# Optimization experiments

Hardware: AMD Instinct MI355X
Metric: run time of the kernel (lower is better)

Reference implementation:

```python
import jax, jax.numpy as jnp
import numpy as np

T, NE, NA, OBS, D, CH, VH, ITERS = 128, 64, 8, 64, 128, 128, 256, 2
B = NE * NA  # num_actors


def setup_inputs() -> dict:
    key = jax.random.key(0)
    ks = jax.random.split(key, 16)
    rn = lambda k, shape, s=0.05: jax.random.normal(k, shape, jnp.float32) * s
    z = lambda *shape: jnp.zeros(shape, jnp.float32)
    return dict(
        hidden=z(B, D),
        obs=rn(ks[0], (T, B, OBS), 1.0),
        dones=jax.random.bernoulli(ks[1], 0.05, (T, B)),
        embed1_w=rn(ks[2], (OBS, D)), embed1_b=z(D),
        embed2_w=rn(ks[3], (D, D)), embed2_b=z(D),
        gru_Wi=rn(ks[4], (D, 3 * D)), gru_bi=z(3 * D),
        gru_Wh=rn(ks[5], (D, 3 * D)), gru_bhn=z(D),
        couple_h_w=rn(ks[6], (2 * D, CH)), couple_h_b=z(CH),
        couple_out_w=rn(ks[7], (CH, 1)), couple_out_b=z(1),
        update_h_w=rn(ks[8], (2 * D, D)), update_h_b=z(D),
        update_out_w=rn(ks[9], (D, D)), update_out_b=z(D),
        value_h1_w=rn(ks[10], (D, VH)), value_h1_b=z(VH),
        value_h2_w=rn(ks[11], (VH, VH)), value_h2_b=z(VH),
        value_out_w=rn(ks[12], (VH, 1)), value_out_b=z(1),
    )


def _gru_scan(hidden, x, dones, Wi, bi, Wh, bhn):
    # flax GRUCell math: r,z gates (no hidden bias), n gate with hidden bias.
    def step(h, xd):
        xt, dt = xd
        h = jnp.where(dt[:, None], 0.0, h)  # reset carry on done
        gi = xt @ Wi + bi                   # [B, 3D]
        gh = h @ Wh                         # [B, 3D]
        i_r, i_z, i_n = jnp.split(gi, 3, axis=-1)
        h_r, h_z, h_n = jnp.split(gh, 3, axis=-1)
        r = jax.nn.sigmoid(i_r + h_r)
        zg = jax.nn.sigmoid(i_z + h_z)
        n = jnp.tanh(i_n + r * (h_n + bhn))
        new_h = (1.0 - zg) * n + zg * h
        return new_h, new_h
    return jax.lax.scan(step, hidden, (x, dones))


def reference(hidden, obs, dones,
              embed1_w, embed1_b, embed2_w, embed2_b,
              gru_Wi, gru_bi, gru_Wh, gru_bhn,
              couple_h_w, couple_h_b, couple_out_w, couple_out_b,
              update_h_w, update_h_b, update_out_w, update_out_b,
              value_h1_w, value_h1_b, value_h2_w, value_h2_b,
              value_out_w, value_out_b):
    # observation embedding MLP
    emb = jax.nn.relu(obs @ embed1_w + embed1_b)
    emb = jax.nn.relu(emb @ embed2_w + embed2_b)
    hidden, rnn_out = _gru_scan(hidden, emb, dones, gru_Wi, gru_bi, gru_Wh, gru_bhn)

    e = rnn_out.reshape(T, NE, NA, D)
    alive = (1.0 - dones.astype(jnp.float32)).reshape(T, NE, NA)
    e = e * alive[..., None]
    identity_mask = 1.0 - jnp.eye(NA, dtype=jnp.float32)

    # split-linear trick: couple_h(concat[h_i, h_j]) == h_i @ W1 + h_j @ W2 + b
    W1, W2 = couple_h_w[:D], couple_h_w[D:]
    U1, U2 = update_h_w[:D], update_h_w[D:]

    for _ in range(ITERS):
        a_i = jnp.einsum('teid,dh->teih', e, W1)  # [T,E,A,CH]
        a_j = jnp.einsum('tejd,dh->tejh', e, W2)
        Ch = jax.nn.relu(a_i[:, :, :, None, :] + a_j[:, :, None, :, :] + couple_h_b)  # [T,E,A,A,CH]
        C = jax.nn.sigmoid(jnp.einsum('teijh,h->teij', Ch, couple_out_w[:, 0]) + couple_out_b[0])
        C = C * alive[:, :, None, :] * identity_mask[None, None, :, :]
        context = jnp.einsum('teij,tejd->teid', C, e)
        delta = jax.nn.relu(e @ U1 + context @ U2 + update_h_b)
        delta = jax.nn.relu(delta @ update_out_w + update_out_b)
        e = (e + delta) * alive[..., None]

    v = jax.nn.relu(e @ value_h1_w + value_h1_b)
    v = jax.nn.relu(v @ value_h2_w + value_h2_b)
    v = (v @ value_out_w + value_out_b)[..., 0]  # [T,E,A]
    values = v.reshape(T, B)
    return hidden, values
```

## Files before the change

### kernel.cpp

```cpp
#include <hip/hip_runtime.h>
#include <hip/hip_bf16.h>
#include <math.h>

#define T_ 128
#define NE_ 64
#define NA_ 8
#define B_ 512
#define OBS_ 64
#define D_ 128
#define CH_ 128
#define VH_ 256
#define M_ (T_*B_)

typedef __attribute__((ext_vector_type(8))) short bf16x8;
typedef __attribute__((ext_vector_type(8))) _Float16 f16x8;
typedef __attribute__((ext_vector_type(4))) float f32x4;

__device__ __forceinline__ float sigmoidf_(float x){ return 1.f/(1.f+__expf(-x)); }
__device__ __forceinline__ unsigned short f2bu(float v){
  __hip_bfloat16 b = __float2bfloat16(v);
  return __builtin_bit_cast(unsigned short, b);
}
__device__ __forceinline__ float bu2f(unsigned short u){
  return __builtin_bit_cast(float, (unsigned int)u << 16);
}
__device__ __forceinline__ unsigned short f2hu(float v){
  _Float16 h = (_Float16)v;
  return __builtin_bit_cast(unsigned short, h);
}
__device__ __forceinline__ float hu2f(unsigned short u){
  return (float)__builtin_bit_cast(_Float16, u);
}

__global__ __launch_bounds__(256)
void embgi_k(const float* __restrict__ obs,
             const ushort* __restrict__ e1wT, const float* __restrict__ e1b,
             const ushort* __restrict__ e2wT, const float* __restrict__ e2b,
             const ushort* __restrict__ gWiT, const float* __restrict__ gbi,
             ushort* __restrict__ giH)
{
  __shared__ ushort S1[128*136];
  __shared__ ushort S2[128*136];
  const int tid  = threadIdx.x;
  const int lane = tid & 63, wave = tid >> 6;
  const int wm = wave >> 1, wn = wave & 1;
  const int quad = lane >> 4, ln = lane & 15;
  const int m0 = blockIdx.x * 128;

  f32x4 acc[4][4];

  #pragma unroll
  for (int i=0;i<8;i++){
    int c4 = tid + i*256;
    int m = c4 >> 4, kf = (c4 & 15) * 4;
    float4 v = *(const float4*)&obs[(size_t)(m0+m)*OBS_ + kf];
    ushort4 h; h.x=f2hu(v.x); h.y=f2hu(v.y); h.z=f2hu(v.z); h.w=f2hu(v.w);
    *(ushort4*)&S1[m*136 + kf] = h;
  }
  #pragma unroll
  for (int i=0;i<4;i++){
    int c8 = tid + i*256;
    int n = c8 >> 3, kq = (c8 & 7)*8;
    *(uint4*)&S2[n*136 + kq] = *(const uint4*)&e1wT[(size_t)n*64 + kq];
  }
  __syncthreads();

  #pragma unroll
  for (int i=0;i<4;i++)
    #pragma unroll
    for (int j=0;j<4;j++)
      #pragma unroll
      for (int r=0;r<4;r++) acc[i][j][r] = 0.f;
  #pragma unroll
  for (int ks=0; ks<2; ks++){
    const int kq = ks*32 + quad*8;
    f16x8 af[4], bfv[4];
    #pragma unroll
    for (int mt=0;mt<4;mt++)
      af[mt] = *(const f16x8*)&S1[(wm*64 + mt*16 + ln)*136 + kq];
    #pragma unroll
    for (int nt=0;nt<4;nt++)
      bfv[nt] = *(const f16x8*)&S2[(wn*64 + nt*16 + ln)*136 + kq];
    #pragma unroll
    for (int mt=0;mt<4;mt++)
      #pragma unroll
      for (int nt=0;nt<4;nt++)
        acc[mt][nt] = __builtin_amdgcn_mfma_f32_16x16x32_f16(af[mt], bfv[nt], acc[mt][nt], 0,0,0);
  }
  __syncthreads();

  #pragma unroll
  for (int mt=0;mt<4;mt++)
    #pragma unroll
    for (int r=0;r<4;r++){
      int rl = wm*64 + mt*16 + quad*4 + r;
      #pragma unroll
      for (int nt=0;nt<4;nt++){
        int cl = wn*64 + nt*16 + ln;
        S1[rl*136 + cl] = f2hu(fmaxf(acc[mt][nt][r] + e1b[cl], 0.f));
      }
    }
  #pragma unroll
  for (int i=0;i<8;i++){
    int c8 = tid + i*256;
    int n = c8 >> 4, kq = (c8 & 15)*8;
    *(uint4*)&S2[n*136 + kq] = *(const uint4*)&e2wT[(size_t)n*128 + kq];
  }
  __syncthreads();

  #pragma unroll
  for (int i=0;i<4;i++)
    #pragma unroll
    for (int j=0;j<4;j++)
      #pragma unroll
      for (int r=0;r<4;r++) acc[i][j][r] = 0.f;
  #pragma unroll
  for (int ks=0; ks<4; ks++){
    const int kq = ks*32 + quad*8;
    f16x8 af[4], bfv[4];
    #pragma unroll
    for (int mt=0;mt<4;mt++)
      af[mt] = *(const f16x8*)&S1[(wm*64 + mt*16 + ln)*136 + kq];
    #pragma unroll
    for (int nt=0;nt<4;nt++)
      bfv[nt] = *(const f16x8*)&S2[(wn*64 + nt*16 + ln)*136 + kq];
    #pragma unroll
    for (int mt=0;mt<4;mt++)
      #pragma unroll
      for (int nt=0;nt<4;nt++)
        acc[mt][nt] = __builtin_amdgcn_mfma_f32_16x16x32_f16(af[mt], bfv[nt], acc[mt][nt], 0,0,0);
  }
  __syncthreads();

  #pragma unroll
  for (int mt=0;mt<4;mt++)
    #pragma unroll
    for (int r=0;r<4;r++){
      int rl = wm*64 + mt*16 + quad*4 + r;
      #pragma unroll
      for (int nt=0;nt<4;nt++){
        int cl = wn*64 + nt*16 + ln;
        S1[rl*136 + cl] = f2hu(fmaxf(acc[mt][nt][r] + e2b[cl], 0.f));
      }
    }

  for (int c=0; c<3; c++){
    #pragma unroll
    for (int i=0;i<8;i++){
      int c8 = tid + i*256;
      int n = c8 >> 4, kq = (c8 & 15)*8;
      *(uint4*)&S2[n*136 + kq] = *(const uint4*)&gWiT[(size_t)(c*128+n)*128 + kq];
    }
    __syncthreads();
    #pragma unroll
    for (int i=0;i<4;i++)
      #pragma unroll
      for (int j=0;j<4;j++)
        #pragma unroll
        for (int r=0;r<4;r++) acc[i][j][r] = 0.f;
    #pragma unroll
    for (int ks=0; ks<4; ks++){
      const int kq = ks*32 + quad*8;
      f16x8 af[4], bfv[4];
      #pragma unroll
      for (int mt=0;mt<4;mt++)
        af[mt] = *(const f16x8*)&S1[(wm*64 + mt*16 + ln)*136 + kq];
      #pragma unroll
      for (int nt=0;nt<4;nt++)
        bfv[nt] = *(const f16x8*)&S2[(wn*64 + nt*16 + ln)*136 + kq];
      #pragma unroll
      for (int mt=0;mt<4;mt++)
        #pragma unroll
        for (int nt=0;nt<4;nt++)
          acc[mt][nt] = __builtin_amdgcn_mfma_f32_16x16x32_f16(af[mt], bfv[nt], acc[mt][nt], 0,0,0);
    }
    __syncthreads();
    #pragma unroll
    for (int mt=0;mt<4;mt++)
      #pragma unroll
      for (int r=0;r<4;r++){
        int row = m0 + wm*64 + mt*16 + quad*4 + r;
        #pragma unroll
        for (int nt=0;nt<4;nt++){
          int cl = wn*64 + nt*16 + ln;
          giH[(size_t)row*384 + c*128 + cl] = f2hu(acc[mt][nt][r] + gbi[c*128 + cl]);
        }
      }
  }
}

__global__ __launch_bounds__(512, 1)
void postgru_k(const __hip_bfloat16* __restrict__ Xe, const __hip_bfloat16* __restrict__ bcatT,
               const float* __restrict__ chb, const float* __restrict__ cow,
               const float* __restrict__ cob,
               const __hip_bfloat16* __restrict__ uhwT, const float* __restrict__ uhb,
               const __hip_bfloat16* __restrict__ uowT, const float* __restrict__ uob,
               const int* __restrict__ dones,
               const __hip_bfloat16* __restrict__ v1wT, const float* __restrict__ v1b,
               const __hip_bfloat16* __restrict__ v2wT, const float* __restrict__ v2b,
               const float* __restrict__ vow, const float* __restrict__ vob,
               float* __restrict__ values)
{
  __shared__ ushort S1[128*136];
  __shared__ ushort Bs[128*136];
  __shared__ alignas(16) ushort Pool[2*128*136];
  __shared__ alignas(16) float cbw[CH_], cww[CH_];
  __shared__ float Cs[4][NA_][NA_];
  __shared__ float SRed[128];
  const int tid  = threadIdx.x;
  const int lane = tid & 63, wave = tid >> 6;
  const int wm = wave >> 1, wn = wave & 1;
  const int quad = lane >> 4, ln = lane & 15;
  const int m0 = blockIdx.x * 128;

  ushort* XcS = Pool;
  float (*AI)[132] = (float(*)[132])(Pool + 128*136);
  float (*AJ)[132] = (float(*)[132])((char*)(Pool + 128*136) + 16896);

  #pragma unroll
  for (int i=0;i<4;i++){
    int c8 = tid + i*512;
    int m = c8 >> 4, kq = (c8 & 15)*8;
    *(uint4*)&S1[m*136 + kq] = *(const uint4*)((const ushort*)Xe + (size_t)(m0+m)*128 + kq);
  }
  if (tid < 128){ cbw[tid] = chb[tid]; cww[tid] = cow[tid]; }
  const float cob0 = cob[0];
  __syncthreads();

  for (int it=0; it<2; it++){
    for (int g=0; g<4; g++){
      const int r0 = g*32;
      const int wrow = wave >> 2;
      const int wcol = wave & 3;

      #pragma unroll
      for (int i=0;i<4;i++){
        int c8 = tid + i*512;
        int n = c8 >> 4, kq = (c8 & 15)*8;
        *(uint4*)&Bs[n*136 + kq] = *(const uint4*)((const ushort*)bcatT + (size_t)n*128 + kq);
      }
      __syncthreads();
      {
        f32x4 accc[2];
        #pragma unroll
        for (int nt=0;nt<2;nt++)
          #pragma unroll
          for (int r=0;r<4;r++) accc[nt][r] = 0.f;
        #pragma unroll
        for (int ks=0; ks<4; ks++){
          const int kq = ks*32 + quad*8;
          bf16x8 af = *(const bf16x8*)&S1[(r0 + wrow*16 + ln)*136 + kq];
          #pragma unroll
          for (int nt=0;nt<2;nt++){
            bf16x8 bfv = *(const bf16x8*)&Bs[(wcol*32 + nt*16 + ln)*136 + kq];
            accc[nt] = __builtin_amdgcn_mfma_f32_16x16x32_bf16(af, bfv, accc[nt], 0,0,0);
          }
        }
        __syncthreads();
        #pragma unroll
        for (int nt=0;nt<2;nt++)
          #pragma unroll
          for (int r=0;r<4;r++)
            AI[wrow*16 + quad*4 + r][wcol*32 + nt*16 + ln] = accc[nt][r];
      }
      #pragma unroll
      for (int i=0;i<4;i++){
        int c8 = tid + i*512;
        int n = c8 >> 4, kq = (c8 & 15)*8;
        *(uint4*)&Bs[n*136 + kq] = *(const uint4*)((const ushort*)bcatT + (size_t)(128+n)*128 + kq);
      }
      __syncthreads();
      {
        f32x4 accc[2];
        #pragma unroll
        for (int nt=0;nt<2;nt++)
          #pragma unroll
          for (int r=0;r<4;r++) accc[nt][r] = 0.f;
        #pragma unroll
        for (int ks=0; ks<4; ks++){
          const int kq = ks*32 + quad*8;
          bf16x8 af = *(const bf16x8*)&S1[(r0 + wrow*16 + ln)*136 + kq];
          #pragma unroll
          for (int nt=0;nt<2;nt++){
            bf16x8 bfv = *(const bf16x8*)&Bs[(wcol*32 + nt*16 + ln)*136 + kq];
            accc[nt] = __builtin_amdgcn_mfma_f32_16x16x32_bf16(af, bfv, accc[nt], 0,0,0);
          }
        }
        #pragma unroll
        for (int nt=0;nt<2;nt++)
          #pragma unroll
          for (int r=0;r<4;r++)
            AJ[wrow*16 + quad*4 + r][wcol*32 + nt*16 + ln] = accc[nt][r];
      }
      __syncthreads();

      {
        const int env = tid >> 7;
        const int i   = (tid >> 4) & 7;
        const int jg  = (tid >> 3) & 1;
        const int hq  = tid & 7;
        const float* aiR = &AI[env*8 + i][0];
        const float* aj0 = &AJ[env*8 + jg*4 + 0][0];
        const float* aj1 = &AJ[env*8 + jg*4 + 1][0];
        const float* aj2 = &AJ[env*8 + jg*4 + 2][0];
        const float* aj3 = &AJ[env*8 + jg*4 + 3][0];
        float s0=0.f, s1=0.f, s2=0.f, s3=0.f;
        #pragma unroll
        for (int t=0; t<4; t++){
          int h = (hq + t*8)*4;
          float4 a4 = *(const float4*)&aiR[h];
          float4 c4 = *(const float4*)&cbw[h];
          float4 w4 = *(const float4*)&cww[h];
          float px = a4.x + c4.x, py = a4.y + c4.y, pz = a4.z + c4.z, pw = a4.w + c4.w;
          float4 b0 = *(const float4*)&aj0[h];
          s0 += fmaxf(px+b0.x,0.f)*w4.x + fmaxf(py+b0.y,0.f)*w4.y
              + fmaxf(pz+b0.z,0.f)*w4.z + fmaxf(pw+b0.w,0.f)*w4.w;
          float4 b1 = *(const float4*)&aj1[h];
          s1 += fmaxf(px+b1.x,0.f)*w4.x + fmaxf(py+b1.y,0.f)*w4.y
              + fmaxf(pz+b1.z,0.f)*w4.z + fmaxf(pw+b1.w,0.f)*w4.w;
          float4 b2 = *(const float4*)&aj2[h];
          s2 += fmaxf(px+b2.x,0.f)*w4.x + fmaxf(py+b2.y,0.f)*w4.y
              + fmaxf(pz+b2.z,0.f)*w4.z + fmaxf(pw+b2.w,0.f)*w4.w;
          float4 b3 = *(const float4*)&aj3[h];
          s3 += fmaxf(px+b3.x,0.f)*w4.x + fmaxf(py+b3.y,0.f)*w4.y
              + fmaxf(pz+b3.z,0.f)*w4.z + fmaxf(pw+b3.w,0.f)*w4.w;
        }
        s0 += __shfl_xor(s0,1); s0 += __shfl_xor(s0,2); s0 += __shfl_xor(s0,4);
        s1 += __shfl_xor(s1,1); s1 += __shfl_xor(s1,2); s1 += __shfl_xor(s1,4);
        s2 += __shfl_xor(s2,1); s2 += __shfl_xor(s2,2); s2 += __shfl_xor(s2,4);
        s3 += __shfl_xor(s3,1); s3 += __shfl_xor(s3,2); s3 += __shfl_xor(s3,4);
        if (hq == 0){
          int j0 = jg*4;
          float c0 = sigmoidf_(s0 + cob0); Cs[env][i][j0+0] = (i==j0+0)?0.f:c0;
          float c1 = sigmoidf_(s1 + cob0); Cs[env][i][j0+1] = (i==j0+1)?0.f:c1;
          float c2 = sigmoidf_(s2 + cob0); Cs[env][i][j0+2] = (i==j0+2)?0.f:c2;
          float c3 = sigmoidf_(s3 + cob0); Cs[env][i][j0+3] = (i==j0+3)?0.f:c3;
        }
      }
      __syncthreads();

      {
        const int lr = tid >> 4;
        const int env = lr >> 3, ii = lr & 7;
        const int c0 = (tid & 15) * 8;
        #pragma unroll
        for (int cc=0; cc<2; cc++){
          int d = c0 + cc*4;
          float a0=0.f, a1=0.f, a2=0.f, a3=0.f;
          #pragma unroll
          for (int j=0;j<NA_;j++){
            float c = Cs[env][ii][j];
            ushort4 e4 = *(const ushort4*)&S1[(r0 + env*8 + j)*136 + d];
            a0 = fmaf(c, bu2f(e4.x), a0);
            a1 = fmaf(c, bu2f(e4.y), a1);
            a2 = fmaf(c, bu2f(e4.z), a2);
            a3 = fmaf(c, bu2f(e4.w), a3);
          }
          ushort4 o; o.x=f2bu(a0); o.y=f2bu(a1); o.z=f2bu(a2); o.w=f2bu(a3);
          *(ushort4*)&XcS[(r0 + lr)*136 + d] = o;
        }
      }
      __syncthreads();
    }

    f32x4 acc[2][4];
    #pragma unroll
    for (int i=0;i<2;i++)
      #pragma unroll
      for (int j=0;j<4;j++)
        #pragma unroll
        for (int r=0;r<4;r++) acc[i][j][r] = 0.f;

    #pragma unroll
    for (int kc=0; kc<2; kc++){
      #pragma unroll
      for (int i=0;i<4;i++){
        int c8 = tid + i*512;
        int n = c8 >> 4, kq = (c8 & 15)*8;
        *(uint4*)&Bs[n*136 + kq] = *(const uint4*)((const ushort*)uhwT + (size_t)n*256 + kc*128 + kq);
      }
      __syncthreads();
      const ushort* Ab = kc ? XcS : S1;
      #pragma unroll
      for (int ks=0; ks<4; ks++){
        const int kq = ks*32 + quad*8;
        bf16x8 af[2], bfv[4];
        #pragma unroll
        for (int mt=0;mt<2;mt++)
          af[mt] = *(const bf16x8*)&Ab[(wm*32 + mt*16 + ln)*136 + kq];
        #pragma unroll
        for (int nt=0;nt<4;nt++)
          bfv[nt] = *(const bf16x8*)&Bs[(wn*64 + nt*16 + ln)*136 + kq];
        #pragma unroll
        for (int mt=0;mt<2;mt++)
          #pragma unroll
          for (int nt=0;nt<4;nt++)
            acc[mt][nt] = __builtin_amdgcn_mfma_f32_16x16x32_bf16(af[mt], bfv[nt], acc[mt][nt], 0,0,0);
      }
      __syncthreads();
    }

    #pragma unroll
    for (int i=0;i<4;i++){
      int c8 = tid + i*512;
      int n = c8 >> 4, kq = (c8 & 15)*8;
      *(uint4*)&Bs[n*136 + kq] = *(const uint4*)((const ushort*)uowT + (size_t)n*128 + kq);
    }
    #pragma unroll
    for (int mt=0;mt<2;mt++)
      #pragma unroll
      for (int r=0;r<4;r++){
        int rl = wm*32 + mt*16 + quad*4 + r;
        #pragma unroll
        for (int nt=0;nt<4;nt++){
          int cl = wn*64 + nt*16 + ln;
          XcS[rl*136 + cl] = f2bu(fmaxf(acc[mt][nt][r] + uhb[cl], 0.f));
        }
      }
    __syncthreads();

    f32x4 acc2[2][4];
    #pragma unroll
    for (int i=0;i<2;i++)
      #pragma unroll
      for (int j=0;j<4;j++)
        #pragma unroll
        for (int r=0;r<4;r++) acc2[i][j][r] = 0.f;
    #pragma unroll
    for (int ks=0; ks<4; ks++){
      const int kq = ks*32 + quad*8;
      bf16x8 af[2], bfv[4];
      #pragma unroll
      for (int mt=0;mt<2;mt++)
        af[mt] = *(const bf16x8*)&XcS[(wm*32 + mt*16 + ln)*136 + kq];
      #pragma unroll
      for (int nt=0;nt<4;nt++)
        bfv[nt] = *(const bf16x8*)&Bs[(wn*64 + nt*16 + ln)*136 + kq];
      #pragma unroll
      for (int mt=0;mt<2;mt++)
        #pragma unroll
        for (int nt=0;nt<4;nt++)
          acc2[mt][nt] = __builtin_amdgcn_mfma_f32_16x16x32_bf16(af[mt], bfv[nt], acc2[mt][nt], 0,0,0);
    }
    #pragma unroll
    for (int mt=0;mt<2;mt++){
      #pragma unroll
      for (int r=0;r<4;r++){
        int rl = wm*32 + mt*16 + quad*4 + r;
        int row = m0 + rl;
        float al = (dones[row]!=0) ? 0.f : 1.f;
        #pragma unroll
        for (int nt=0;nt<4;nt++){
          int cl = wn*64 + nt*16 + ln;
          float v = fmaxf(acc2[mt][nt][r] + uob[cl], 0.f);
          v += bu2f(S1[rl*136 + cl]);
          v *= al;
          S1[rl*136 + cl] = f2bu(v);
        }
      }
    }
    __syncthreads();
  }

  ushort* V1 = Pool;

  for (int h=0; h<2; h++){
    #pragma unroll
    for (int i=0;i<4;i++){
      int c8 = tid + i*512;
      int n = c8 >> 4, kq = (c8 & 15)*8;
      *(uint4*)&Bs[n*136 + kq] = *(const uint4*)((const ushort*)v1wT + (size_t)(h*128+n)*128 + kq);
    }
    __syncthreads();
    f32x4 acc[2][4];
    #pragma unroll
    for (int i=0;i<2;i++)
      #pragma unroll
      for (int j=0;j<4;j++)
        #pragma unroll
        for (int r=0;r<4;r++) acc[i][j][r] = 0.f;
    #pragma unroll
    for (int ks=0; ks<4; ks++){
      const int kq = ks*32 + quad*8;
      bf16x8 af[2], bfv[4];
      #pragma unroll
      for (int mt=0;mt<2;mt++)
        af[mt] = *(const bf16x8*)&S1[(wm*32 + mt*16 + ln)*136 + kq];
      #pragma unroll
      for (int nt=0;nt<4;nt++)
        bfv[nt] = *(const bf16x8*)&Bs[(wn*64 + nt*16 + ln)*136 + kq];
      #pragma unroll
      for (int mt=0;mt<2;mt++)
        #pragma unroll
        for (int nt=0;nt<4;nt++)
          acc[mt][nt] = __builtin_amdgcn_mfma_f32_16x16x32_bf16(af[mt], bfv[nt], acc[mt][nt], 0,0,0);
    }
    __syncthreads();
    #pragma unroll
    for (int mt=0;mt<2;mt++)
      #pragma unroll
      for (int r=0;r<4;r++){
        int rl = wm*32 + mt*16 + quad*4 + r;
        #pragma unroll
        for (int nt=0;nt<4;nt++){
          int cl = wn*64 + nt*16 + ln;
          V1[h*128*136 + rl*136 + cl] = f2bu(fmaxf(acc[mt][nt][r] + v1b[h*128 + cl], 0.f));
        }
      }
  }

  float s[2][4];
  #pragma unroll
  for (int mt=0;mt<2;mt++)
    #pragma unroll
    for (int r=0;r<4;r++) s[mt][r] = 0.f;

  for (int oc=0; oc<2; oc++){
    f32x4 acc[2][4];
    #pragma unroll
    for (int i=0;i<2;i++)
      #pragma unroll
      for (int j=0;j<4;j++)
        #pragma unroll
        for (int r=0;r<4;r++) acc[i][j][r] = 0.f;
    for (int kh=0; kh<2; kh++){
      #pragma unroll
      for (int i=0;i<4;i++){
        int c8 = tid + i*512;
        int n = c8 >> 4, kq = (c8 & 15)*8;
        *(uint4*)&Bs[n*136 + kq] = *(const uint4*)((const ushort*)v2wT + (size_t)(oc*128+n)*256 + kh*128 + kq);
      }
      __syncthreads();
      #pragma unroll
      for (int ks=0; ks<4; ks++){
        const int kq = ks*32 + quad*8;
        bf16x8 af[2], bfv[4];
        #pragma unroll
        for (int mt=0;mt<2;mt++)
          af[mt] = *(const bf16x8*)&V1[kh*128*136 + (wm*32 + mt*16 + ln)*136 + kq];
        #pragma unroll
        for (int nt=0;nt<4;nt++)
          bfv[nt] = *(const bf16x8*)&Bs[(wn*64 + nt*16 + ln)*136 + kq];
        #pragma unroll
        for (int mt=0;mt<2;mt++)
          #pragma unroll
          for (int nt=0;nt<4;nt++)
            acc[mt][nt] = __builtin_amdgcn_mfma_f32_16x16x32_bf16(af[mt], bfv[nt], acc[mt][nt], 0,0,0);
      }
      __syncthreads();
    }
    float v2bv[4], voww[4];
    #pragma unroll
    for (int nt=0;nt<4;nt++){
      int col = oc*128 + wn*64 + nt*16 + ln;
      v2bv[nt] = v2b[col];
      voww[nt] = vow[col];
    }
    #pragma unroll
    for (int mt=0;mt<2;mt++)
      #pragma unroll
      for (int r=0;r<4;r++){
        float p = 0.f;
        #pragma unroll
        for (int nt=0;nt<4;nt++)
          p += fmaxf(acc[mt][nt][r] + v2bv[nt], 0.f) * voww[nt];
        s[mt][r] += p;
      }
  }

  #pragma unroll
  for (int off=1; off<16; off<<=1)
    #pragma unroll
    for (int mt=0;mt<2;mt++)
      #pragma unroll
      for (int r=0;r<4;r++)
        s[mt][r] += __shfl_xor(s[mt][r], off);
  if (ln == 0 && wn == 1){
    #pragma unroll
    for (int mt=0;mt<2;mt++)
      #pragma unroll
      for (int r=0;r<4;r++)
        SRed[wm*32 + mt*16 + quad*4 + r] = s[mt][r];
  }
  __syncthreads();
  if (ln == 0 && wn == 0){
    float vob0 = vob[0];
    #pragma unroll
    for (int mt=0;mt<2;mt++)
      #pragma unroll
      for (int r=0;r<4;r++){
        int rl = wm*32 + mt*16 + quad*4 + r;
        values[m0 + rl] = s[mt][r] + SRed[rl] + vob0;
      }
  }
}

__global__ __launch_bounds__(512, 1)
void grum8_k(const ushort* __restrict__ gih, const float* __restrict__ hidden0,
             const int* __restrict__ dones, const float* __restrict__ gWh,
             const float* __restrict__ bhn, __hip_bfloat16* __restrict__ eb_out,
             float* __restrict__ hout)
{
  __shared__ ushort wstg[32*392];
  __shared__ ushort hb[2][16*136];
  __shared__ float  dnS[T_*4];
  const int tid  = threadIdx.x;
  const int lane = tid & 63, wave = tid >> 6;
  const int quad = lane >> 4, ln = lane & 15;
  const int r0   = blockIdx.x * 4;
  const int col  = wave*16 + ln;
  const int lnb  = ln & 12;

  dnS[tid] = (dones[(size_t)(tid>>2)*B_ + r0 + (tid&3)] != 0) ? 1.f : 0.f;
  const float bhnr = bhn[col];

  for (int i=tid; i<16*136; i+=512){ hb[0][i]=0; hb[1][i]=0; }

  f16x8 bf[3][4];
  #pragma unroll
  for (int kc=0; kc<4; kc++){
    for (int i=tid; i<32*384; i+=512){
      int kk = i/384, c = i - kk*384;
      wstg[kk*392 + c] = f2hu(gWh[(size_t)(kc*32+kk)*384 + c]);
    }
    __syncthreads();
    #pragma unroll
    for (int g=0; g<3; g++){
      int c = g*128 + col;
      ushort tmp[8];
      #pragma unroll
      for (int j=0;j<8;j++) tmp[j] = wstg[(quad*8+j)*392 + c];
      bf[g][kc] = *(const f16x8*)tmp;
    }
    __syncthreads();
  }

  float hc = hidden0[(size_t)(r0+quad)*D_ + col];
  if (dnS[quad] > 0.5f) hc = 0.f;
  hb[0][(quad*4)*136 + col] = f2hu(hc);
  __syncthreads();

  const ushort* gbase = gih + ((size_t)(r0+quad))*384;
  const size_t  gstep = (size_t)B_*384;

  float c_r, c_z, c_n;
  c_r = hu2f(gbase[col]); c_z = hu2f(gbase[col+128]); c_n = hu2f(gbase[col+256]);
  ushort aR,aZ,aN, bR,bZ,bN, cR,cZ,cN, dR,dZ,dN;
  { const ushort* gp = gbase + 1*gstep; aR = gp[col]; aZ = gp[col+128]; aN = gp[col+256]; }
  { const ushort* gp = gbase + 2*gstep; bR = gp[col]; bZ = gp[col+128]; bN = gp[col+256]; }
  { const ushort* gp = gbase + 3*gstep; cR = gp[col]; cZ = gp[col+128]; cN = gp[col+256]; }
  dR=0; dZ=0; dN=0;

  ushort pend_eu = 0;

#define GSTEP(t, IR,IZ,IN, OR,OZ,ON)                                          \
  {                                                                           \
    if ((t) > 0)                                                              \
      ((ushort*)eb_out)[((size_t)((t)-1)*B_ + r0+quad)*D_ + col] = pend_eu;   \
    { int tl = (t)+4; if (tl > T_-1) tl = T_-1;                               \
      const ushort* gp = gbase + (size_t)tl*gstep;                            \
      OR = gp[col]; OZ = gp[col+128]; ON = gp[col+256]; }                     \
    const ushort* hbuf = hb[(t)&1];                                           \
    f32x4 accA[3], accB[3];                                                   \
    _Pragma("unroll")                                                         \
    for (int g=0;g<3;g++){                                                    \
      _Pragma("unroll")                                                       \
      for (int r=0;r<4;r++){ accA[g][r]=0.f; accB[g][r]=0.f; }                \
    }                                                                         \
    _Pragma("unroll")                                                         \
    for (int ks=0; ks<2; ks++){                                               \
      f16x8 ahA = *(const f16x8*)&hbuf[lnb*136 + (2*ks  )*32 + quad*8];       \
      f16x8 ahB = *(const f16x8*)&hbuf[lnb*136 + (2*ks+1)*32 + quad*8];       \
      _Pragma("unroll")                                                       \
      for (int g=0;g<3;g++){                                                  \
        accA[g] = __builtin_amdgcn_mfma_f32_16x16x32_f16(ahA, bf[g][2*ks  ], accA[g], 0,0,0); \
        accB[g] = __builtin_amdgcn_mfma_f32_16x16x32_f16(ahB, bf[g][2*ks+1], accB[g], 0,0,0); \
      }                                                                       \
    }                                                                         \
    const float dnow  = dnS[(t)*4 + quad];                                    \
    const float dnext = ((t)+1 < T_) ? dnS[((t)+1)*4 + quad] : 0.f;           \
    float rg = sigmoidf_(c_r + accA[0][0] + accB[0][0]);                      \
    float zg = sigmoidf_(c_z + accA[1][0] + accB[1][0]);                      \
    float x  = c_n + rg*(accA[2][0] + accB[2][0] + bhnr);                     \
    float ng = 2.f/(1.f+__expf(-2.f*x)) - 1.f;                                \
    float hnew = (1.f - zg)*ng + zg*hc;                                       \
    pend_eu = f2bu(hnew*(1.f-dnow));                                          \
    float hv = (dnext > 0.5f) ? 0.f : hnew;                                   \
    hc = hv;                                                                  \
    hb[((t)+1)&1][(quad*4)*136 + col] = f2hu(hv);                             \
    asm volatile("s_waitcnt lgkmcnt(0)\n\ts_barrier" ::: "memory");           \
    c_r = hu2f(IR); c_z = hu2f(IZ); c_n = hu2f(IN);                           \
  }

  for (int t=0; t<T_; t+=4){
    GSTEP(t+0, aR,aZ,aN, dR,dZ,dN);
    GSTEP(t+1, bR,bZ,bN, aR,aZ,aN);
    GSTEP(t+2, cR,cZ,cN, bR,bZ,bN);
    GSTEP(t+3, dR,dZ,dN, cR,cZ,cN);
  }
#undef GSTEP

  ((ushort*)eb_out)[((size_t)(T_-1)*B_ + r0+quad)*D_ + col] = pend_eu;
  hout[(size_t)(r0+quad)*D_ + col] = hc;
}

__global__ __launch_bounds__(256)
void packall_k(const float* __restrict__ e1w, ushort* __restrict__ e1T,
               const float* __restrict__ e2w, ushort* __restrict__ e2T,
               const float* __restrict__ gWi, ushort* __restrict__ giT,
               const float* __restrict__ chw, __hip_bfloat16* __restrict__ bcatT,
               const float* __restrict__ uhw, __hip_bfloat16* __restrict__ uhwT,
               const float* __restrict__ uow, __hip_bfloat16* __restrict__ uowT,
               const float* __restrict__ v1w, __hip_bfloat16* __restrict__ v1wT,
               const float* __restrict__ v2w, __hip_bfloat16* __restrict__ v2wT)
{
  const int b = blockIdx.x, tid = threadIdx.x;
  if (b < 32){
    int idx = b*256 + tid;
    int n = idx >> 6, k = idx & 63;
    e1T[idx] = f2hu(e1w[k*128 + n]);
  } else if (b < 96){
    int idx = (b-32)*256 + tid;
    int n = idx >> 7, k = idx & 127;
    e2T[idx] = f2hu(e2w[k*128 + n]);
  } else if (b < 288){
    int idx = (b-96)*256 + tid;
    int n = idx >> 7, k = idx & 127;
    giT[idx] = f2hu(gWi[k*384 + n]);
  } else if (b < 416){
    int idx = (b-288)*256 + tid;
    int n = idx >> 7, k = idx & 127;
    float v = (n < 128) ? chw[k*128 + n] : chw[(128+k)*128 + (n-128)];
    bcatT[idx] = __float2bfloat16(v);
  } else if (b < 544){
    int idx = (b-416)*256 + tid;
    int r = idx >> 7, c = idx & 127;
    uhwT[c*256 + r] = __float2bfloat16(uhw[idx]);
  } else if (b < 608){
    int idx = (b-544)*256 + tid;
    int r = idx >> 7, c = idx & 127;
    uowT[c*128 + r] = __float2bfloat16(uow[idx]);
  } else if (b < 736){
    int idx = (b-608)*256 + tid;
    int r = idx >> 8, c = idx & 255;
    v1wT[c*128 + r] = __float2bfloat16(v1w[idx]);
  } else {
    int idx = (b-736)*256 + tid;
    int r = idx >> 8, c = idx & 255;
    v2wT[c*256 + r] = __float2bfloat16(v2w[idx]);
  }
}

extern "C" void kernel_launch(void* const* d_in, const int* in_sizes, int n_in,
                              void* d_out, int out_size, void* d_ws, size_t ws_size,
                              hipStream_t stream) {
  const float* hidden = (const float*)d_in[0];
  const float* obs    = (const float*)d_in[1];
  const int*   dones  = (const int*)  d_in[2];
  const float* e1w = (const float*)d_in[3];
  const float* e1b = (const float*)d_in[4];
  const float* e2w = (const float*)d_in[5];
  const float* e2b = (const float*)d_in[6];
  const float* gWi = (const float*)d_in[7];
  const float* gbi = (const float*)d_in[8];
  const float* gWh = (const float*)d_in[9];
  const float* gbhn= (const float*)d_in[10];
  const float* chw = (const float*)d_in[11];
  const float* chb = (const float*)d_in[12];
  const float* cow = (const float*)d_in[13];
  const float* cob = (const float*)d_in[14];
  const float* uhw = (const float*)d_in[15];
  const float* uhb = (const float*)d_in[16];
  const float* uow = (const float*)d_in[17];
  const float* uob = (const float*)d_in[18];
  const float* v1w = (const float*)d_in[19];
  const float* v1b = (const float*)d_in[20];
  const float* v2w = (const float*)d_in[21];
  const float* v2b = (const float*)d_in[22];
  const float* vow = (const float*)d_in[23];
  const float* vob = (const float*)d_in[24];
  (void)in_sizes; (void)n_in; (void)out_size;

  float* out_hidden = (float*)d_out;
  float* out_values = (float*)d_out + (size_t)B_*D_;

  float* ws = (float*)d_ws;
  ushort* giH   = (ushort*)(ws + 10485760);
  __hip_bfloat16* Xe = (__hip_bfloat16*)(ws + 23068672);
  ushort* wb    = (ushort*)(ws + 27262976);
  if (ws_size < (size_t)27500000 * sizeof(float)) return;

  __hip_bfloat16* bcatT = (__hip_bfloat16*)wb;
  __hip_bfloat16* uhwT  = (__hip_bfloat16*)wb + 32768;
  __hip_bfloat16* uowT  = (__hip_bfloat16*)wb + 65536;
  __hip_bfloat16* v1wT  = (__hip_bfloat16*)wb + 81920;
  __hip_bfloat16* v2wT  = (__hip_bfloat16*)wb + 114688;
  ushort* e1wT = wb + 180224;
  ushort* e2wT = wb + 188416;
  ushort* gWiT = wb + 204800;

  dim3 blk(256);
  packall_k<<<dim3(992), blk, 0, stream>>>(
    e1w, e1wT, e2w, e2wT, gWi, gWiT,
    chw, bcatT, uhw, uhwT, uow, uowT, v1w, v1wT, v2w, v2wT);

  embgi_k<<<dim3(512), blk, 0, stream>>>(obs, e1wT, e1b, e2wT, e2b, gWiT, gbi, giH);

  grum8_k<<<dim3(128), dim3(512), 0, stream>>>(giH, hidden, dones, gWh, gbhn, Xe, out_hidden);

  postgru_k<<<dim3(512), dim3(512), 0, stream>>>(Xe, bcatT, chb, cow, cob,
                                                 uhwT, uhb, uowT, uob, dones,
                                                 v1wT, v1b, v2wT, v2b, vow, vob, out_values);
}
```

Measured before the change: 309.8 us.

## Double postgru_k block to 1024 threads and repartition work across 16 waves

The post-GRU kernel now launches 1024 threads per block instead of 512. Every GEMM tile, coupling-score loop, context loop and final reduction is remapped so each wave holds half the accumulators. The goal is more latency hiding and parallelism within the 128-row block, since only 512 blocks run with one block per CU. In exchange, the barriers are shared by more waves and register pressure per thread is tighter under the 1024 launch bound.

```diff
diff --git a/kernel.cpp b/kernel.cpp
--- a/kernel.cpp
+++ b/kernel.cpp
@@ -189,7 +189,7 @@
   }
 }
 
-__global__ __launch_bounds__(512, 1)
+__global__ __launch_bounds__(1024, 1)
 void postgru_k(const __hip_bfloat16* __restrict__ Xe, const __hip_bfloat16* __restrict__ bcatT,
                const float* __restrict__ chb, const float* __restrict__ cow,
                const float* __restrict__ cob,
@@ -206,10 +206,10 @@
   __shared__ alignas(16) ushort Pool[2*128*136];
   __shared__ alignas(16) float cbw[CH_], cww[CH_];
   __shared__ float Cs[4][NA_][NA_];
-  __shared__ float SRed[128];
+  __shared__ float SRedP[4][128];
   const int tid  = threadIdx.x;
   const int lane = tid & 63, wave = tid >> 6;
-  const int wm = wave >> 1, wn = wave & 1;
+  const int wm = wave >> 2, wn = wave & 3;
   const int quad = lane >> 4, ln = lane & 15;
   const int m0 = blockIdx.x * 128;
 
@@ -218,8 +218,8 @@
   float (*AJ)[132] = (float(*)[132])((char*)(Pool + 128*136) + 16896);
 
   #pragma unroll
-  for (int i=0;i<4;i++){
-    int c8 = tid + i*512;
+  for (int i=0;i<2;i++){
+    int c8 = tid + i*1024;
     int m = c8 >> 4, kq = (c8 & 15)*8;
     *(uint4*)&S1[m*136 + kq] = *(const uint4*)((const ushort*)Xe + (size_t)(m0+m)*128 + kq);
   }
@@ -230,152 +230,118 @@
   for (int it=0; it<2; it++){
     for (int g=0; g<4; g++){
       const int r0 = g*32;
-      const int wrow = wave >> 2;
-      const int wcol = wave & 3;
-
-      #pragma unroll
-      for (int i=0;i<4;i++){
-        int c8 = tid + i*512;
+      const int wrow = wave >> 3;
+      const int wcol = wave & 7;
+
+      #pragma unroll
+      for (int i=0;i<2;i++){
+        int c8 = tid + i*1024;
         int n = c8 >> 4, kq = (c8 & 15)*8;
         *(uint4*)&Bs[n*136 + kq] = *(const uint4*)((const ushort*)bcatT + (size_t)n*128 + kq);
       }
       __syncthreads();
       {
-        f32x4 accc[2];
-        #pragma unroll
-        for (int nt=0;nt<2;nt++)
-          #pragma unroll
-          for (int r=0;r<4;r++) accc[nt][r] = 0.f;
+        f32x4 accc;
+        #pragma unroll
+        for (int r=0;r<4;r++) accc[r] = 0.f;
         #pragma unroll
         for (int ks=0; ks<4; ks++){
           const int kq = ks*32 + quad*8;
-          bf16x8 af = *(const bf16x8*)&S1[(r0 + wrow*16 + ln)*136 + kq];
-          #pragma unroll
-          for (int nt=0;nt<2;nt++){
-            bf16x8 bfv = *(const bf16x8*)&Bs[(wcol*32 + nt*16 + ln)*136 + kq];
-            accc[nt] = __builtin_amdgcn_mfma_f32_16x16x32_bf16(af, bfv, accc[nt], 0,0,0);
-          }
+          bf16x8 af  = *(const bf16x8*)&S1[(r0 + wrow*16 + ln)*136 + kq];
+          bf16x8 bfv = *(const bf16x8*)&Bs[(wcol*16 + ln)*136 + kq];
+          accc = __builtin_amdgcn_mfma_f32_16x16x32_bf16(af, bfv, accc, 0,0,0);
         }
         __syncthreads();
         #pragma unroll
-        for (int nt=0;nt<2;nt++)
-          #pragma unroll
-          for (int r=0;r<4;r++)
-            AI[wrow*16 + quad*4 + r][wcol*32 + nt*16 + ln] = accc[nt][r];
-      }
-      #pragma unroll
-      for (int i=0;i<4;i++){
-        int c8 = tid + i*512;
+        for (int r=0;r<4;r++)
+          AI[wrow*16 + quad*4 + r][wcol*16 + ln] = accc[r];
+      }
+      #pragma unroll
+      for (int i=0;i<2;i++){
+        int c8 = tid + i*1024;
         int n = c8 >> 4, kq = (c8 & 15)*8;
         *(uint4*)&Bs[n*136 + kq] = *(const uint4*)((const ushort*)bcatT + (size_t)(128+n)*128 + kq);
       }
       __syncthreads();
       {
-        f32x4 accc[2];
-        #pragma unroll
-        for (int nt=0;nt<2;nt++)
-          #pragma unroll
-          for (int r=0;r<4;r++) accc[nt][r] = 0.f;
+        f32x4 accc;
+        #pragma unroll
+        for (int r=0;r<4;r++) accc[r] = 0.f;
         #pragma unroll
         for (int ks=0; ks<4; ks++){
           const int kq = ks*32 + quad*8;
-          bf16x8 af = *(const bf16x8*)&S1[(r0 + wrow*16 + ln)*136 + kq];
-          #pragma unroll
-          for (int nt=0;nt<2;nt++){
-            bf16x8 bfv = *(const bf16x8*)&Bs[(wcol*32 + nt*16 + ln)*136 + kq];
-            accc[nt] = __builtin_amdgcn_mfma_f32_16x16x32_bf16(af, bfv, accc[nt], 0,0,0);
-          }
-        }
-        #pragma unroll
-        for (int nt=0;nt<2;nt++)
-          #pragma unroll
-          for (int r=0;r<4;r++)
-            AJ[wrow*16 + quad*4 + r][wcol*32 + nt*16 + ln] = accc[nt][r];
+          bf16x8 af  = *(const bf16x8*)&S1[(r0 + wrow*16 + ln)*136 + kq];
+          bf16x8 bfv = *(const bf16x8*)&Bs[(wcol*16 + ln)*136 + kq];
+          accc = __builtin_amdgcn_mfma_f32_16x16x32_bf16(af, bfv, accc, 0,0,0);
+        }
+        #pragma unroll
+        for (int r=0;r<4;r++)
+          AJ[wrow*16 + quad*4 + r][wcol*16 + ln] = accc[r];
       }
       __syncthreads();
 
       {
-        const int env = tid >> 7;
-        const int i   = (tid >> 4) & 7;
-        const int jg  = (tid >> 3) & 1;
-        const int hq  = tid & 7;
+        const int env = tid >> 8;
+        const int i   = (tid >> 5) & 7;
+        const int j   = (tid >> 2) & 7;
+        const int hq  = tid & 3;
         const float* aiR = &AI[env*8 + i][0];
-        const float* aj0 = &AJ[env*8 + jg*4 + 0][0];
-        const float* aj1 = &AJ[env*8 + jg*4 + 1][0];
-        const float* aj2 = &AJ[env*8 + jg*4 + 2][0];
-        const float* aj3 = &AJ[env*8 + jg*4 + 3][0];
-        float s0=0.f, s1=0.f, s2=0.f, s3=0.f;
-        #pragma unroll
-        for (int t=0; t<4; t++){
-          int h = (hq + t*8)*4;
+        const float* ajR = &AJ[env*8 + j][0];
+        float s = 0.f;
+        #pragma unroll
+        for (int t=0; t<8; t++){
+          int h = (hq + t*4)*4;
           float4 a4 = *(const float4*)&aiR[h];
+          float4 b4 = *(const float4*)&ajR[h];
           float4 c4 = *(const float4*)&cbw[h];
           float4 w4 = *(const float4*)&cww[h];
-          float px = a4.x + c4.x, py = a4.y + c4.y, pz = a4.z + c4.z, pw = a4.w + c4.w;
-          float4 b0 = *(const float4*)&aj0[h];
-          s0 += fmaxf(px+b0.x,0.f)*w4.x + fmaxf(py+b0.y,0.f)*w4.y
-              + fmaxf(pz+b0.z,0.f)*w4.z + fmaxf(pw+b0.w,0.f)*w4.w;
-          float4 b1 = *(const float4*)&aj1[h];
-          s1 += fmaxf(px+b1.x,0.f)*w4.x + fmaxf(py+b1.y,0.f)*w4.y
-              + fmaxf(pz+b1.z,0.f)*w4.z + fmaxf(pw+b1.w,0.f)*w4.w;
-          float4 b2 = *(const float4*)&aj2[h];
-          s2 += fmaxf(px+b2.x,0.f)*w4.x + fmaxf(py+b2.y,0.f)*w4.y
-              + fmaxf(pz+b2.z,0.f)*w4.z + fmaxf(pw+b2.w,0.f)*w4.w;
-          float4 b3 = *(const float4*)&aj3[h];
-          s3 += fmaxf(px+b3.x,0.f)*w4.x + fmaxf(py+b3.y,0.f)*w4.y
-              + fmaxf(pz+b3.z,0.f)*w4.z + fmaxf(pw+b3.w,0.f)*w4.w;
-        }
-        s0 += __shfl_xor(s0,1); s0 += __shfl_xor(s0,2); s0 += __shfl_xor(s0,4);
-        s1 += __shfl_xor(s1,1); s1 += __shfl_xor(s1,2); s1 += __shfl_xor(s1,4);
-        s2 += __shfl_xor(s2,1); s2 += __shfl_xor(s2,2); s2 += __shfl_xor(s2,4);
-        s3 += __shfl_xor(s3,1); s3 += __shfl_xor(s3,2); s3 += __shfl_xor(s3,4);
+          s += fmaxf(a4.x + b4.x + c4.x, 0.f) * w4.x
+             + fmaxf(a4.y + b4.y + c4.y, 0.f) * w4.y
+             + fmaxf(a4.z + b4.z + c4.z, 0.f) * w4.z
+             + fmaxf(a4.w + b4.w + c4.w, 0.f) * w4.w;
+        }
+        s += __shfl_xor(s, 1);
+        s += __shfl_xor(s, 2);
         if (hq == 0){
-          int j0 = jg*4;
-          float c0 = sigmoidf_(s0 + cob0); Cs[env][i][j0+0] = (i==j0+0)?0.f:c0;
-          float c1 = sigmoidf_(s1 + cob0); Cs[env][i][j0+1] = (i==j0+1)?0.f:c1;
-          float c2 = sigmoidf_(s2 + cob0); Cs[env][i][j0+2] = (i==j0+2)?0.f:c2;
-          float c3 = sigmoidf_(s3 + cob0); Cs[env][i][j0+3] = (i==j0+3)?0.f:c3;
+          float Cv = sigmoidf_(s + cob0);
+          Cs[env][i][j] = (i==j) ? 0.f : Cv;
         }
       }
       __syncthreads();
 
       {
-        const int lr = tid >> 4;
+        const int lr = tid >> 5;
         const int env = lr >> 3, ii = lr & 7;
-        const int c0 = (tid & 15) * 8;
-        #pragma unroll
-        for (int cc=0; cc<2; cc++){
-          int d = c0 + cc*4;
-          float a0=0.f, a1=0.f, a2=0.f, a3=0.f;
-          #pragma unroll
-          for (int j=0;j<NA_;j++){
-            float c = Cs[env][ii][j];
-            ushort4 e4 = *(const ushort4*)&S1[(r0 + env*8 + j)*136 + d];
-            a0 = fmaf(c, bu2f(e4.x), a0);
-            a1 = fmaf(c, bu2f(e4.y), a1);
-            a2 = fmaf(c, bu2f(e4.z), a2);
-            a3 = fmaf(c, bu2f(e4.w), a3);
-          }
-          ushort4 o; o.x=f2bu(a0); o.y=f2bu(a1); o.z=f2bu(a2); o.w=f2bu(a3);
-          *(ushort4*)&XcS[(r0 + lr)*136 + d] = o;
-        }
-      }
-      __syncthreads();
-    }
-
-    f32x4 acc[2][4];
+        const int d = (tid & 31) * 4;
+        float a0=0.f, a1=0.f, a2=0.f, a3=0.f;
+        #pragma unroll
+        for (int j=0;j<NA_;j++){
+          float c = Cs[env][ii][j];
+          ushort4 e4 = *(const ushort4*)&S1[(r0 + env*8 + j)*136 + d];
+          a0 = fmaf(c, bu2f(e4.x), a0);
+          a1 = fmaf(c, bu2f(e4.y), a1);
+          a2 = fmaf(c, bu2f(e4.z), a2);
+          a3 = fmaf(c, bu2f(e4.w), a3);
+        }
+        ushort4 o; o.x=f2bu(a0); o.y=f2bu(a1); o.z=f2bu(a2); o.w=f2bu(a3);
+        *(ushort4*)&XcS[(r0 + lr)*136 + d] = o;
+      }
+      __syncthreads();
+    }
+
+    f32x4 acc[2][2];
     #pragma unroll
     for (int i=0;i<2;i++)
       #pragma unroll
-      for (int j=0;j<4;j++)
+      for (int j=0;j<2;j++)
         #pragma unroll
         for (int r=0;r<4;r++) acc[i][j][r] = 0.f;
 
     #pragma unroll
     for (int kc=0; kc<2; kc++){
       #pragma unroll
-      for (int i=0;i<4;i++){
-        int c8 = tid + i*512;
+      for (int i=0;i<2;i++){
+        int c8 = tid + i*1024;
         int n = c8 >> 4, kq = (c8 & 15)*8;
         *(uint4*)&Bs[n*136 + kq] = *(const uint4*)((const ushort*)uhwT + (size_t)n*256 + kc*128 + kq);
       }
@@ -384,25 +350,25 @@
       #pragma unroll
       for (int ks=0; ks<4; ks++){
         const int kq = ks*32 + quad*8;
-        bf16x8 af[2], bfv[4];
+        bf16x8 af[2], bfv[2];
         #pragma unroll
         for (int mt=0;mt<2;mt++)
           af[mt] = *(const bf16x8*)&Ab[(wm*32 + mt*16 + ln)*136 + kq];
         #pragma unroll
-        for (int nt=0;nt<4;nt++)
-          bfv[nt] = *(const bf16x8*)&Bs[(wn*64 + nt*16 + ln)*136 + kq];
+        for (int nt=0;nt<2;nt++)
+          bfv[nt] = *(const bf16x8*)&Bs[(wn*32 + nt*16 + ln)*136 + kq];
         #pragma unroll
         for (int mt=0;mt<2;mt++)
           #pragma unroll
-          for (int nt=0;nt<4;nt++)
+          for (int nt=0;nt<2;nt++)
             acc[mt][nt] = __builtin_amdgcn_mfma_f32_16x16x32_bf16(af[mt], bfv[nt], acc[mt][nt], 0,0,0);
       }
       __syncthreads();
     }
 
     #pragma unroll
-    for (int i=0;i<4;i++){
-      int c8 = tid + i*512;
+    for (int i=0;i<2;i++){
+      int c8 = tid + i*1024;
       int n = c8 >> 4, kq = (c8 & 15)*8;
       *(uint4*)&Bs[n*136 + kq] = *(const uint4*)((const ushort*)uowT + (size_t)n*128 + kq);
     }
@@ -412,34 +378,34 @@
       for (int r=0;r<4;r++){
         int rl = wm*32 + mt*16 + quad*4 + r;
         #pragma unroll
-        for (int nt=0;nt<4;nt++){
-          int cl = wn*64 + nt*16 + ln;
+        for (int nt=0;nt<2;nt++){
+          int cl = wn*32 + nt*16 + ln;
           XcS[rl*136 + cl] = f2bu(fmaxf(acc[mt][nt][r] + uhb[cl], 0.f));
         }
       }
     __syncthreads();
 
-    f32x4 acc2[2][4];
+    f32x4 acc2[2][2];
     #pragma unroll
     for (int i=0;i<2;i++)
       #pragma unroll
-      for (int j=0;j<4;j++)
+      for (int j=0;j<2;j++)
         #pragma unroll
         for (int r=0;r<4;r++) acc2[i][j][r] = 0.f;
     #pragma unroll
     for (int ks=0; ks<4; ks++){
       const int kq = ks*32 + quad*8;
-      bf16x8 af[2], bfv[4];
+      bf16x8 af[2], bfv[2];
       #pragma unroll
       for (int mt=0;mt<2;mt++)
         af[mt] = *(const bf16x8*)&XcS[(wm*32 + mt*16 + ln)*136 + kq];
       #pragma unroll
-      for (int nt=0;nt<4;nt++)
-        bfv[nt] = *(const bf16x8*)&Bs[(wn*64 + nt*16 + ln)*136 + kq];
+      for (int nt=0;nt<2;nt++)
+        bfv[nt] = *(const bf16x8*)&Bs[(wn*32 + nt*16 + ln)*136 + kq];
       #pragma unroll
       for (int mt=0;mt<2;mt++)
         #pragma unroll
-        for (int nt=0;nt<4;nt++)
+        for (int nt=0;nt<2;nt++)
           acc2[mt][nt] = __builtin_amdgcn_mfma_f32_16x16x32_bf16(af[mt], bfv[nt], acc2[mt][nt], 0,0,0);
     }
     #pragma unroll
@@ -450,8 +416,8 @@
         int row = m0 + rl;
         float al = (dones[row]!=0) ? 0.f : 1.f;
         #pragma unroll
-        for (int nt=0;nt<4;nt++){
-          int cl = wn*64 + nt*16 + ln;
+        for (int nt=0;nt<2;nt++){
+          int cl = wn*32 + nt*16 + ln;
           float v = fmaxf(acc2[mt][nt][r] + uob[cl], 0.f);
           v += bu2f(S1[rl*136 + cl]);
           v *= al;
@@ -466,33 +432,33 @@
 
   for (int h=0; h<2; h++){
     #pragma unroll
-    for (int i=0;i<4;i++){
-      int c8 = tid + i*512;
+    for (int i=0;i<2;i++){
+      int c8 = tid + i*1024;
       int n = c8 >> 4, kq = (c8 & 15)*8;
       *(uint4*)&Bs[n*136 + kq] = *(const uint4*)((const ushort*)v1wT + (size_t)(h*128+n)*128 + kq);
     }
     __syncthreads();
-    f32x4 acc[2][4];
+    f32x4 acc[2][2];
     #pragma unroll
     for (int i=0;i<2;i++)
       #pragma unroll
-      for (int j=0;j<4;j++)
+      for (int j=0;j<2;j++)
         #pragma unroll
         for (int r=0;r<4;r++) acc[i][j][r] = 0.f;
     #pragma unroll
     for (int ks=0; ks<4; ks++){
       const int kq = ks*32 + quad*8;
-      bf16x8 af[2], bfv[4];
+      bf16x8 af[2], bfv[2];
       #pragma unroll
       for (int mt=0;mt<2;mt++)
         af[mt] = *(const bf16x8*)&S1[(wm*32 + mt*16 + ln)*136 + kq];
       #pragma unroll
-      for (int nt=0;nt<4;nt++)
-        bfv[nt] = *(const bf16x8*)&Bs[(wn*64 + nt*16 + ln)*136 + kq];
+      for (int nt=0;nt<2;nt++)
+        bfv[nt] = *(const bf16x8*)&Bs[(wn*32 + nt*16 + ln)*136 + kq];
       #pragma unroll
       for (int mt=0;mt<2;mt++)
         #pragma unroll
-        for (int nt=0;nt<4;nt++)
+        for (int nt=0;nt<2;nt++)
           acc[mt][nt] = __builtin_amdgcn_mfma_f32_16x16x32_bf16(af[mt], bfv[nt], acc[mt][nt], 0,0,0);
     }
     __syncthreads();
@@ -502,8 +468,8 @@
       for (int r=0;r<4;r++){
         int rl = wm*32 + mt*16 + quad*4 + r;
         #pragma unroll
-        for (int nt=0;nt<4;nt++){
-          int cl = wn*64 + nt*16 + ln;
+        for (int nt=0;nt<2;nt++){
+          int cl = wn*32 + nt*16 + ln;
           V1[h*128*136 + rl*136 + cl] = f2bu(fmaxf(acc[mt][nt][r] + v1b[h*128 + cl], 0.f));
         }
       }
@@ -516,17 +482,17 @@
     for (int r=0;r<4;r++) s[mt][r] = 0.f;
 
   for (int oc=0; oc<2; oc++){
-    f32x4 acc[2][4];
+    f32x4 acc[2][2];
     #pragma unroll
     for (int i=0;i<2;i++)
       #pragma unroll
-      for (int j=0;j<4;j++)
+      for (int j=0;j<2;j++)
         #pragma unroll
         for (int r=0;r<4;r++) acc[i][j][r] = 0.f;
     for (int kh=0; kh<2; kh++){
       #pragma unroll
-      for (int i=0;i<4;i++){
-        int c8 = tid + i*512;
+      for (int i=0;i<2;i++){
+        int c8 = tid + i*1024;
         int n = c8 >> 4, kq = (c8 & 15)*8;
         *(uint4*)&Bs[n*136 + kq] = *(const uint4*)((const ushort*)v2wT + (size_t)(oc*128+n)*256 + kh*128 + kq);
       }
@@ -534,25 +500,25 @@
       #pragma unroll
       for (int ks=0; ks<4; ks++){
         const int kq = ks*32 + quad*8;
-        bf16x8 af[2], bfv[4];
+        bf16x8 af[2], bfv[2];
         #pragma unroll
         for (int mt=0;mt<2;mt++)
           af[mt] = *(const bf16x8*)&V1[kh*128*136 + (wm*32 + mt*16 + ln)*136 + kq];
         #pragma unroll
-        for (int nt=0;nt<4;nt++)
-          bfv[nt] = *(const bf16x8*)&Bs[(wn*64 + nt*16 + ln)*136 + kq];
+        for (int nt=0;nt<2;nt++)
+          bfv[nt] = *(const bf16x8*)&Bs[(wn*32 + nt*16 + ln)*136 + kq];
         #pragma unroll
         for (int mt=0;mt<2;mt++)
           #pragma unroll
-          for (int nt=0;nt<4;nt++)
+          for (int nt=0;nt<2;nt++)
             acc[mt][nt] = __builtin_amdgcn_mfma_f32_16x16x32_bf16(af[mt], bfv[nt], acc[mt][nt], 0,0,0);
       }
       __syncthreads();
     }
-    float v2bv[4], voww[4];
-    #pragma unroll
-    for (int nt=0;nt<4;nt++){
-      int col = oc*128 + wn*64 + nt*16 + ln;
+    float v2bv[2], voww[2];
+    #pragma unroll
+    for (int nt=0;nt<2;nt++){
+      int col = oc*128 + wn*32 + nt*16 + ln;
       v2bv[nt] = v2b[col];
       voww[nt] = vow[col];
     }
@@ -562,7 +528,7 @@
       for (int r=0;r<4;r++){
         float p = 0.f;
         #pragma unroll
-        for (int nt=0;nt<4;nt++)
+        for (int nt=0;nt<2;nt++)
           p += fmaxf(acc[mt][nt][r] + v2bv[nt], 0.f) * voww[nt];
         s[mt][r] += p;
       }
@@ -575,23 +541,16 @@
       #pragma unroll
       for (int r=0;r<4;r++)
         s[mt][r] += __shfl_xor(s[mt][r], off);
-  if (ln == 0 && wn == 1){
+  if (ln == 0){
     #pragma unroll
     for (int mt=0;mt<2;mt++)
       #pragma unroll
       for (int r=0;r<4;r++)
-        SRed[wm*32 + mt*16 + quad*4 + r] = s[mt][r];
+        SRedP[wn][wm*32 + mt*16 + quad*4 + r] = s[mt][r];
   }
   __syncthreads();
-  if (ln == 0 && wn == 0){
-    float vob0 = vob[0];
-    #pragma unroll
-    for (int mt=0;mt<2;mt++)
-      #pragma unroll
-      for (int r=0;r<4;r++){
-        int rl = wm*32 + mt*16 + quad*4 + r;
-        values[m0 + rl] = s[mt][r] + SRed[rl] + vob0;
-      }
+  if (tid < 128){
+    values[m0 + tid] = SRedP[0][tid] + SRedP[1][tid] + SRedP[2][tid] + SRedP[3][tid] + vob[0];
   }
 }
 
@@ -808,7 +767,7 @@
 
   grum8_k<<<dim3(128), dim3(512), 0, stream>>>(giH, hidden, dones, gWh, gbhn, Xe, out_hidden);
 
-  postgru_k<<<dim3(512), dim3(512), 0, stream>>>(Xe, bcatT, chb, cow, cob,
-                                                 uhwT, uhb, uowT, uob, dones,
-                                                 v1wT, v1b, v2wT, v2b, vow, vob, out_values);
-}
+  postgru_k<<<dim3(512), dim3(1024), 0, stream>>>(Xe, bcatT, chb, cow, cob,
+                                                  uhwT, uhb, uowT, uob, dones,
+                                                  v1wT, v1b, v2wT, v2b, vow, vob, out_values);
+}
```

New measurement: 321.7 us. 3.8% more time.
